# Optimization experiments

Hardware: AMD Instinct MI355X
Metric: run time of the kernel (lower is better)

The kernel has to match this reference:

```python
import jax, jax.numpy as jnp
import numpy as np

B, S, D, H = 2, 2048, 1024, 16
DH = D // H  # per-head depth = 64


def setup_inputs() -> dict:
    key = jax.random.key(0)
    ks = jax.random.split(key, 10)
    s = 1.0 / np.sqrt(D)
    return {
        "q_in": jax.random.normal(ks[0], (B, S, D), jnp.float32),
        "k_in": jax.random.normal(ks[1], (B, S, D), jnp.float32),
        "v_in": jax.random.normal(ks[2], (B, S, D), jnp.float32),
        "mask": jnp.zeros((B, 1, S, S), jnp.float32),
        "Wq": jax.random.normal(ks[3], (D, D), jnp.float32) * s,
        "bq": jnp.zeros((D,), jnp.float32),
        "Wk": jax.random.normal(ks[4], (D, D), jnp.float32) * s,
        "bk": jnp.zeros((D,), jnp.float32),
        "Wv": jax.random.normal(ks[5], (D, D), jnp.float32) * s,
        "bv": jnp.zeros((D,), jnp.float32),
        "Wo": jax.random.normal(ks[6], (D, D), jnp.float32) * s,
        "bo": jnp.zeros((D,), jnp.float32),
    }


def _split_heads(x):
    # [B,S,D] -> [B,H,S,DH]
    b, s, _ = x.shape
    return x.reshape(b, s, H, DH).transpose(0, 2, 1, 3)


def reference(q_in, k_in, v_in, mask, Wq, bq, Wk, bk, Wv, bv, Wo, bo):
    q = _split_heads(q_in @ Wq + bq)
    k = _split_heads(k_in @ Wk + bk)
    v = _split_heads(v_in @ Wv + bv)
    logits = jnp.einsum("bhqd,bhkd->bhqk", q, k) / jnp.sqrt(jnp.float32(DH))
    logits = logits + mask * -1e9
    attn = jax.nn.softmax(logits, axis=-1)
    ctx = jnp.einsum("bhqk,bhkd->bhqd", attn, v)  # [B,H,S,DH]
    concat = ctx.transpose(0, 2, 1, 3).reshape(q_in.shape[0], -1, D)
    out = concat @ Wo + bo  # dropout is identity at inference
    return out, attn
```

## Files before the change

kernel.cpp:

```cpp
#include <hip/hip_runtime.h>
#include <hip/hip_bf16.h>

static constexpr int cB = 2, cS = 2048, cD = 1024, cH = 16, cDH = 64;

typedef __attribute__((ext_vector_type(4))) float f32x4;
typedef __attribute__((ext_vector_type(8))) short s16x8;
typedef unsigned long long u64;
typedef unsigned short u16;

__device__ inline f32x4 mfma16(s16x8 a, s16x8 b, f32x4 c) {
  return __builtin_amdgcn_mfma_f32_16x16x32_bf16(a, b, c, 0, 0, 0);
}

__device__ inline u16 f2bf(float x) {
  unsigned u = __float_as_uint(x);
  u += 0x7FFFu + ((u >> 16) & 1u);
  return (u16)(u >> 16);
}

__device__ inline unsigned cvt_pk_bf16(float lo, float hi) {
  unsigned r;
  asm("v_cvt_pk_bf16_f32 %0, %1, %2" : "=v"(r) : "v"(lo), "v"(hi));
  return r;
}

__device__ inline f32x4 zero4() { f32x4 z; z[0] = z[1] = z[2] = z[3] = 0.f; return z; }

__device__ inline void gload16(const void* src, void* dst) {
  __builtin_amdgcn_global_load_lds((const __attribute__((address_space(1))) void*)src,
                                   (__attribute__((address_space(3))) void*)dst, 16, 0, 0);
}

__global__ __launch_bounds__(256) void wt4_kernel(const float* __restrict__ W0,
                                                  const float* __restrict__ W1,
                                                  const float* __restrict__ W2,
                                                  const float* __restrict__ W3,
                                                  u16* __restrict__ T0, u16* __restrict__ T1,
                                                  u16* __restrict__ T2, u16* __restrict__ T3) {
  __shared__ float tile[32][33];
  int z = blockIdx.z;
  const float* W = z == 0 ? W0 : z == 1 ? W1 : z == 2 ? W2 : W3;
  u16* Wt = z == 0 ? T0 : z == 1 ? T1 : z == 2 ? T2 : T3;
  int tx = threadIdx.x, ty = threadIdx.y;
  int r0 = blockIdx.y * 32, c0 = blockIdx.x * 32;
  for (int i = ty; i < 32; i += 8)
    tile[i][tx] = W[(size_t)(r0 + i) * cD + c0 + tx];
  __syncthreads();
  for (int i = ty; i < 32; i += 8)
    Wt[(size_t)(c0 + i) * cD + r0 + tx] = f2bf(tile[tx][i]);
}

__global__ __launch_bounds__(256) void maskflag_kernel(const float* __restrict__ mask,
                                                       unsigned char* __restrict__ flags) {
  int blk = blockIdx.x;
  int b = blk >> 10, qt = (blk >> 5) & 31, kt = blk & 31;
  int t = threadIdx.x;
  int r = t >> 2, c0 = (t & 3) * 16;
  const float4* p = (const float4*)(mask + ((size_t)b * cS + qt * 64 + r) * cS + kt * 64 + c0);
  int any = 0;
  for (int j = 0; j < 4; ++j) {
    float4 v = p[j];
    any |= (v.x != 0.f) | (v.y != 0.f) | (v.z != 0.f) | (v.w != 0.f);
  }
  __shared__ int sred;
  if (t == 0) sred = 0;
  __syncthreads();
  if (any) atomicOr(&sred, 1);
  __syncthreads();
  if (t == 0) flags[blk] = (unsigned char)sred;
}

template<bool AFP32, bool OUTF32, int BN>
__device__ __forceinline__ void gemm_body(const void* __restrict__ Ap,
                                          const u16* __restrict__ Bt,
                                          const float* __restrict__ bias,
                                          void* __restrict__ outp,
                                          float scale, int vt_mode, int bidx,
                                          u16* As, u16* Bs) {
  constexpr int NI = BN / 32;
  constexpr int RPW = BN / 4;
  int t = threadIdx.x;
  int w = t >> 6, l = t & 63, g = l >> 4, li = l & 15;
  int bm = bidx & 31, bn = bidx >> 5;
  int m0 = bm * 128, n0 = bn * BN;
  int wr = w >> 1, wc = w & 1;

  f32x4 acc[4][NI];
  for (int i = 0; i < 4; ++i)
    for (int j = 0; j < NI; ++j) acc[i][j] = zero4();

  for (int kk = 0; kk < cD; kk += 64) {
    if (AFP32) {
      const float* X = (const float*)Ap;
      int ar = t >> 1, ak0 = (t & 1) * 32;
      const float* asrc = X + (size_t)(m0 + ar) * cD + kk + ak0;
      int sw = ar & 7;
      for (int j = 0; j < 4; ++j) {
        float4 x0 = ((const float4*)asrc)[2 * j];
        float4 x1 = ((const float4*)asrc)[2 * j + 1];
        union { s16x8 v; u16 h[8]; } s;
        s.h[0] = f2bf(x0.x); s.h[1] = f2bf(x0.y); s.h[2] = f2bf(x0.z); s.h[3] = f2bf(x0.w);
        s.h[4] = f2bf(x1.x); s.h[5] = f2bf(x1.y); s.h[6] = f2bf(x1.z); s.h[7] = f2bf(x1.w);
        int chunk = (ak0 >> 3) + j;
        *(s16x8*)&As[ar * 64 + ((chunk ^ sw) * 8)] = s.v;
      }
    } else {
      const u16* X = (const u16*)Ap;
      for (int is = 0; is < 4; ++is) {
        int row = w * 32 + is * 8 + (l >> 3);
        int chunk = l & 7;
        const u16* src = X + (size_t)(m0 + row) * cD + kk + ((chunk ^ (row & 7)) * 8);
        gload16(src, &As[(w * 32 + is * 8) * 64]);
      }
    }
    for (int is = 0; is < RPW / 8; ++is) {
      int row = w * RPW + is * 8 + (l >> 3);
      int chunk = l & 7;
      const u16* src = Bt + (size_t)(n0 + row) * cD + kk + ((chunk ^ (row & 7)) * 8);
      gload16(src, &Bs[(w * RPW + is * 8) * 64]);
    }
    __syncthreads();
    for (int c = 0; c < 2; ++c) {
      s16x8 af[4], bf[NI];
      for (int mi = 0; mi < 4; ++mi) {
        int r = wr * 64 + mi * 16 + li;
        af[mi] = *(const s16x8*)&As[r * 64 + (((c * 4 + g) ^ (r & 7)) * 8)];
      }
      for (int ni = 0; ni < NI; ++ni) {
        int r = wc * (BN / 2) + ni * 16 + li;
        bf[ni] = *(const s16x8*)&Bs[r * 64 + (((c * 4 + g) ^ (r & 7)) * 8)];
      }
      for (int mi = 0; mi < 4; ++mi)
        for (int ni = 0; ni < NI; ++ni)
          acc[mi][ni] = mfma16(af[mi], bf[ni], acc[mi][ni]);
    }
    __syncthreads();
  }

  for (int ni = 0; ni < NI; ++ni) {
    int n = n0 + wc * (BN / 2) + ni * 16 + li;
    float bv = bias[n];
    for (int mi = 0; mi < 4; ++mi) {
      for (int r = 0; r < 4; ++r) {
        int m = m0 + wr * 64 + mi * 16 + g * 4 + r;
        float val = acc[mi][ni][r] + bv;
        if (OUTF32) {
          ((float*)outp)[(size_t)m * cD + n] = val;
        } else {
          val *= scale;
          int b = m >> 11, s = m & 2047;
          int h = n >> 6, d = n & 63;
          size_t idx = vt_mode ? ((size_t)(b * cH + h) * cDH + d) * cS + s
                               : ((size_t)(b * cH + h) * cS + s) * cDH + d;
          ((u16*)outp)[idx] = f2bf(val);
        }
      }
    }
  }
}

__global__ __launch_bounds__(256) void qkv_gemm(const float* __restrict__ Xq,
                                                const float* __restrict__ Xk,
                                                const float* __restrict__ Xv,
                                                const u16* __restrict__ Btq,
                                                const u16* __restrict__ Btk,
                                                const u16* __restrict__ Btv,
                                                const float* __restrict__ bq,
                                                const float* __restrict__ bk,
                                                const float* __restrict__ bv,
                                                u16* __restrict__ oq,
                                                u16* __restrict__ ok,
                                                u16* __restrict__ ov) {
  __shared__ __attribute__((aligned(16))) u16 As[128 * 64];
  __shared__ __attribute__((aligned(16))) u16 Bs[128 * 64];
  int which = blockIdx.x >> 8, bidx = blockIdx.x & 255;
  const float* X = which == 0 ? Xq : which == 1 ? Xk : Xv;
  const u16* Bt = which == 0 ? Btq : which == 1 ? Btk : Btv;
  const float* bias = which == 0 ? bq : which == 1 ? bk : bv;
  u16* o = which == 0 ? oq : which == 1 ? ok : ov;
  float scale = which == 0 ? 0.125f : 1.0f;
  int vt = which == 2 ? 1 : 0;
  gemm_body<true, false, 128>(X, Bt, bias, o, scale, vt, bidx, As, Bs);
}

__global__ __launch_bounds__(256) void out_gemm(const u16* __restrict__ Xc,
                                                const u16* __restrict__ Bt,
                                                const float* __restrict__ bias,
                                                float* __restrict__ outp) {
  __shared__ __attribute__((aligned(16))) u16 As[128 * 64];
  __shared__ __attribute__((aligned(16))) u16 Bs[64 * 64];
  gemm_body<false, true, 64>(Xc, Bt, bias, outp, 1.0f, 0, blockIdx.x, As, Bs);
}

__global__ __launch_bounds__(512) void attn_kernel(const u16* __restrict__ Q,
                                                   const u16* __restrict__ K,
                                                   const u16* __restrict__ Vt,
                                                   const float* __restrict__ mask,
                                                   const unsigned char* __restrict__ flags,
                                                   float* __restrict__ attn,
                                                   u16* __restrict__ ctx) {
  __shared__ __attribute__((aligned(16))) u16 Kl[64 * 64];
  __shared__ __attribute__((aligned(16))) u16 Vl[64 * 64];
  int t = threadIdx.x;
  int w = t >> 6, l = t & 63, g = l >> 4, li = l & 15;
  int p = blockIdx.x;
  int blk = (p & 7) * 64 + (p >> 3);
  int bh = blk >> 4, qt = blk & 15;
  int b = bh >> 4;
  int qbase = qt * 128;
  const u16* Qh = Q + (size_t)bh * cS * cDH;
  const u16* Kh = K + (size_t)bh * cS * cDH;
  const u16* Vh = Vt + (size_t)bh * cDH * cS;
  const unsigned char* fl = flags + (b << 10) + ((qbase + w * 16) >> 6) * 32;

  s16x8 qf[2];
  {
    const u16* qp = Qh + (size_t)(qbase + w * 16 + li) * cDH;
    qf[0] = *(const s16x8*)(qp + 8 * g);
    qf[1] = *(const s16x8*)(qp + 32 + 8 * g);
  }
  int srow8 = l >> 3, schunk = l & 7;
  int q_lane = qbase + w * 16 + li;

  float racc = 0.f;
  for (int kt = 0; kt < 32; ++kt) {
    {
      int row = w * 8 + srow8;
      gload16(Kh + (size_t)(kt * 64 + row) * cDH + ((schunk ^ (row & 7)) * 8),
              &Kl[(w * 8) * 64]);
    }
    __syncthreads();
    f32x4 acc[4];
    for (int mt = 0; mt < 4; ++mt) acc[mt] = zero4();
    for (int c = 0; c < 2; ++c)
      for (int mt = 0; mt < 4; ++mt) {
        int r = mt * 16 + li;
        s16x8 kf = *(const s16x8*)&Kl[r * 64 + (((c * 4 + g) ^ (r & 7)) * 8)];
        acc[mt] = mfma16(kf, qf[c], acc[mt]);
      }
    bool um = fl[kt] != 0;
    for (int mt = 0; mt < 4; ++mt)
      for (int r = 0; r < 4; ++r) {
        float lv = acc[mt][r];
        if (um) lv += mask[((size_t)b * cS + q_lane) * cS + kt * 64 + mt * 16 + 4 * g + r] * -1e9f;
        racc += __expf(lv);
      }
    __syncthreads();
  }
  racc += __shfl_xor(racc, 16, 64);
  racc += __shfl_xor(racc, 32, 64);
  float lr = __logf(racc);

  f32x4 cacc[4];
  for (int dt = 0; dt < 4; ++dt) cacc[dt] = zero4();
  float* attn_row = attn + (size_t)bh * cS * cS + (size_t)q_lane * cS;
  for (int kt = 0; kt < 32; ++kt) {
    {
      int row = w * 8 + srow8;
      gload16(Kh + (size_t)(kt * 64 + row) * cDH + ((schunk ^ (row & 7)) * 8),
              &Kl[(w * 8) * 64]);
      gload16(Vh + (size_t)row * cS + kt * 64 + ((schunk ^ (row & 7)) * 8),
              &Vl[(w * 8) * 64]);
    }
    __syncthreads();
    f32x4 acc[4];
    for (int mt = 0; mt < 4; ++mt) acc[mt] = zero4();
    for (int c = 0; c < 2; ++c)
      for (int mt = 0; mt < 4; ++mt) {
        int r = mt * 16 + li;
        s16x8 kf = *(const s16x8*)&Kl[r * 64 + (((c * 4 + g) ^ (r & 7)) * 8)];
        acc[mt] = mfma16(kf, qf[c], acc[mt]);
      }
    bool um = fl[kt] != 0;
    s16x8 pa[2];
    for (int c = 0; c < 2; ++c) {
      union { s16x8 v; unsigned u[4]; } pk;
      f32x4 pvq[2];
      for (int hh = 0; hh < 2; ++hh) {
        int mt = c * 2 + hh;
        for (int r = 0; r < 4; ++r) {
          float lv = acc[mt][r];
          if (um) lv += mask[((size_t)b * cS + q_lane) * cS + kt * 64 + mt * 16 + 4 * g + r] * -1e9f;
          pvq[hh][r] = __expf(lv - lr);
        }
        __builtin_nontemporal_store(pvq[hh], (f32x4*)(attn_row + kt * 64 + mt * 16 + 4 * g));
      }
      pk.u[0] = cvt_pk_bf16(pvq[0][0], pvq[0][1]);
      pk.u[1] = cvt_pk_bf16(pvq[0][2], pvq[0][3]);
      pk.u[2] = cvt_pk_bf16(pvq[1][0], pvq[1][1]);
      pk.u[3] = cvt_pk_bf16(pvq[1][2], pvq[1][3]);
      pa[c] = pk.v;
    }
    for (int c = 0; c < 2; ++c) {
      for (int dt = 0; dt < 4; ++dt) {
        int row = dt * 16 + li;
        const u16* rb = &Vl[row * 64];
        int o0 = (((c * 4 + 0 + (g >> 1)) ^ (li & 7)) * 8) + (g & 1) * 4;
        int o1 = (((c * 4 + 2 + (g >> 1)) ^ (li & 7)) * 8) + (g & 1) * 4;
        union { s16x8 v; u64 qq[2]; } vf;
        vf.qq[0] = *(const u64*)(rb + o0);
        vf.qq[1] = *(const u64*)(rb + o1);
        cacc[dt] = mfma16(pa[c], vf.v, cacc[dt]);
      }
    }
    __syncthreads();
  }

  int h = bh & 15;
  for (int dt = 0; dt < 4; ++dt)
    for (int r = 0; r < 4; ++r) {
      int s = qbase + w * 16 + g * 4 + r;
      int d = dt * 16 + li;
      ctx[((size_t)(b * cS + s)) * cD + h * 64 + d] = f2bf(cacc[dt][r]);
    }
}

extern "C" void kernel_launch(void* const* d_in, const int* in_sizes, int n_in,
                              void* d_out, int out_size, void* d_ws, size_t ws_size,
                              hipStream_t stream) {
  const float* q_in = (const float*)d_in[0];
  const float* k_in = (const float*)d_in[1];
  const float* v_in = (const float*)d_in[2];
  const float* mask = (const float*)d_in[3];
  const float* Wq = (const float*)d_in[4];
  const float* bq = (const float*)d_in[5];
  const float* Wk = (const float*)d_in[6];
  const float* bk = (const float*)d_in[7];
  const float* Wv = (const float*)d_in[8];
  const float* bv = (const float*)d_in[9];
  const float* Wo = (const float*)d_in[10];
  const float* bo = (const float*)d_in[11];

  float* out = (float*)d_out;
  float* attn = out + (size_t)cB * cS * cD;

  const size_t MATB = (size_t)cB * cS * cD * 2;
  const size_t WB = (size_t)cD * cD * 2;
  char* ws = (char*)d_ws;
  u16* WqT = (u16*)(ws);
  u16* WkT = (u16*)(ws + WB);
  u16* WvT = (u16*)(ws + 2 * WB);
  u16* WoT = (u16*)(ws + 3 * WB);
  u16* wsQ  = (u16*)(ws + 4 * WB);
  u16* wsK  = (u16*)(ws + 4 * WB + MATB);
  u16* wsVt = (u16*)(ws + 4 * WB + 2 * MATB);
  u16* wsC  = (u16*)(ws + 4 * WB + 3 * MATB);
  unsigned char* flags = (unsigned char*)(ws + 4 * WB + 4 * MATB);
  const size_t REQUIRED = 4 * WB + 4 * MATB + 2048;
  if (ws_size < REQUIRED) return;

  dim3 tb(32, 8);
  wt4_kernel<<<dim3(32, 32, 4), tb, 0, stream>>>(Wq, Wk, Wv, Wo, WqT, WkT, WvT, WoT);
  maskflag_kernel<<<2048, 256, 0, stream>>>(mask, flags);

  qkv_gemm<<<768, 256, 0, stream>>>(q_in, k_in, v_in, WqT, WkT, WvT,
                                    bq, bk, bv, wsQ, wsK, wsVt);

  attn_kernel<<<512, 512, 0, stream>>>(wsQ, wsK, wsVt, mask, flags, attn, wsC);

  out_gemm<<<512, 256, 0, stream>>>(wsC, WoT, bo, out);
}
```

Baseline: 336.0 us.

## Double-buffer K/V LDS tiles in attention to prefetch the next tile during compute

Splits the attention kernel's K and V shared-memory tiles into two buffers. Both the row-sum pass and the output pass now issue the load for tile kt+1 before computing on tile kt, and replace the two __syncthreads per iteration with a single explicit vmcnt wait plus barrier. The aim is to hide global-to-LDS load latency and cut barrier stalls. In exchange, LDS use doubles and correctness depends on hand-tuned vmcnt counts, for example vmcnt(4) to skip past the outstanding nontemporal attn stores.

```diff
diff --git a/kernel.cpp b/kernel.cpp
--- a/kernel.cpp
+++ b/kernel.cpp
@@ -199,8 +199,8 @@
                                                    const unsigned char* __restrict__ flags,
                                                    float* __restrict__ attn,
                                                    u16* __restrict__ ctx) {
-  __shared__ __attribute__((aligned(16))) u16 Kl[64 * 64];
-  __shared__ __attribute__((aligned(16))) u16 Vl[64 * 64];
+  __shared__ __attribute__((aligned(16))) u16 Kl[2][64 * 64];
+  __shared__ __attribute__((aligned(16))) u16 Vl[2][64 * 64];
   int t = threadIdx.x;
   int w = t >> 6, l = t & 63, g = l >> 4, li = l & 15;
   int p = blockIdx.x;
@@ -221,21 +221,29 @@
   }
   int srow8 = l >> 3, schunk = l & 7;
   int q_lane = qbase + w * 16 + li;
-
+  int srow = w * 8 + srow8;
+  const u16* kstage = Kh + (size_t)srow * cDH + ((schunk ^ (srow & 7)) * 8);
+  const u16* vstage = Vh + (size_t)srow * cS + ((schunk ^ (srow & 7)) * 8);
+  u16* kl_dst = &Kl[0][(w * 8) * 64];
+  u16* vl_dst = &Vl[0][(w * 8) * 64];
+  const int KSTEP = 64 * cDH;
+
+  gload16(kstage, kl_dst);
+  asm volatile("s_waitcnt vmcnt(0)" ::: "memory");
+  __builtin_amdgcn_sched_barrier(0);
+  __builtin_amdgcn_s_barrier();
+  __builtin_amdgcn_sched_barrier(0);
   float racc = 0.f;
   for (int kt = 0; kt < 32; ++kt) {
-    {
-      int row = w * 8 + srow8;
-      gload16(Kh + (size_t)(kt * 64 + row) * cDH + ((schunk ^ (row & 7)) * 8),
-              &Kl[(w * 8) * 64]);
-    }
-    __syncthreads();
+    int cur = kt & 1;
+    if (kt + 1 < 32)
+      gload16(kstage + (size_t)(kt + 1) * KSTEP, kl_dst + (cur ^ 1) * 64 * 64);
     f32x4 acc[4];
     for (int mt = 0; mt < 4; ++mt) acc[mt] = zero4();
     for (int c = 0; c < 2; ++c)
       for (int mt = 0; mt < 4; ++mt) {
         int r = mt * 16 + li;
-        s16x8 kf = *(const s16x8*)&Kl[r * 64 + (((c * 4 + g) ^ (r & 7)) * 8)];
+        s16x8 kf = *(const s16x8*)&Kl[cur][r * 64 + (((c * 4 + g) ^ (r & 7)) * 8)];
         acc[mt] = mfma16(kf, qf[c], acc[mt]);
       }
     bool um = fl[kt] != 0;
@@ -245,7 +253,12 @@
         if (um) lv += mask[((size_t)b * cS + q_lane) * cS + kt * 64 + mt * 16 + 4 * g + r] * -1e9f;
         racc += __expf(lv);
       }
-    __syncthreads();
+    if (kt + 1 < 32) {
+      asm volatile("s_waitcnt vmcnt(0)" ::: "memory");
+      __builtin_amdgcn_sched_barrier(0);
+      __builtin_amdgcn_s_barrier();
+      __builtin_amdgcn_sched_barrier(0);
+    }
   }
   racc += __shfl_xor(racc, 16, 64);
   racc += __shfl_xor(racc, 32, 64);
@@ -254,21 +267,24 @@
   f32x4 cacc[4];
   for (int dt = 0; dt < 4; ++dt) cacc[dt] = zero4();
   float* attn_row = attn + (size_t)bh * cS * cS + (size_t)q_lane * cS;
+  gload16(kstage, kl_dst);
+  gload16(vstage, vl_dst);
+  asm volatile("s_waitcnt vmcnt(0)" ::: "memory");
+  __builtin_amdgcn_sched_barrier(0);
+  __builtin_amdgcn_s_barrier();
+  __builtin_amdgcn_sched_barrier(0);
   for (int kt = 0; kt < 32; ++kt) {
-    {
-      int row = w * 8 + srow8;
-      gload16(Kh + (size_t)(kt * 64 + row) * cDH + ((schunk ^ (row & 7)) * 8),
-              &Kl[(w * 8) * 64]);
-      gload16(Vh + (size_t)row * cS + kt * 64 + ((schunk ^ (row & 7)) * 8),
-              &Vl[(w * 8) * 64]);
-    }
-    __syncthreads();
+    int cur = kt & 1;
+    if (kt + 1 < 32) {
+      gload16(kstage + (size_t)(kt + 1) * KSTEP, kl_dst + (cur ^ 1) * 64 * 64);
+      gload16(vstage + (kt + 1) * 64, vl_dst + (cur ^ 1) * 64 * 64);
+    }
     f32x4 acc[4];
     for (int mt = 0; mt < 4; ++mt) acc[mt] = zero4();
     for (int c = 0; c < 2; ++c)
       for (int mt = 0; mt < 4; ++mt) {
         int r = mt * 16 + li;
-        s16x8 kf = *(const s16x8*)&Kl[r * 64 + (((c * 4 + g) ^ (r & 7)) * 8)];
+        s16x8 kf = *(const s16x8*)&Kl[cur][r * 64 + (((c * 4 + g) ^ (r & 7)) * 8)];
         acc[mt] = mfma16(kf, qf[c], acc[mt]);
       }
     bool um = fl[kt] != 0;
@@ -294,7 +310,7 @@
     for (int c = 0; c < 2; ++c) {
       for (int dt = 0; dt < 4; ++dt) {
         int row = dt * 16 + li;
-        const u16* rb = &Vl[row * 64];
+        const u16* rb = &Vl[cur][row * 64];
         int o0 = (((c * 4 + 0 + (g >> 1)) ^ (li & 7)) * 8) + (g & 1) * 4;
         int o1 = (((c * 4 + 2 + (g >> 1)) ^ (li & 7)) * 8) + (g & 1) * 4;
         union { s16x8 v; u64 qq[2]; } vf;
@@ -303,7 +319,12 @@
         cacc[dt] = mfma16(pa[c], vf.v, cacc[dt]);
       }
     }
-    __syncthreads();
+    if (kt + 1 < 32) {
+      asm volatile("s_waitcnt vmcnt(4)" ::: "memory");
+      __builtin_amdgcn_sched_barrier(0);
+      __builtin_amdgcn_s_barrier();
+      __builtin_amdgcn_sched_barrier(0);
+    }
   }
 
   int h = bh & 15;
```

Result: no change. 334.1 us (-0.6%).
